# Kernel tuning notes

Measured on AMD Instinct MI355X. Metric: run time of the kernel, lower is better.

Reference implementation:

```python
import jax, jax.numpy as jnp
import numpy as np

HID = 128


def _mlp(f, W1, b1, W2, b2, W3, b3):
    h = jax.nn.relu(f @ W1 + b1)
    h = jax.nn.relu(h @ W2 + b2)
    return h @ W3 + b3


def setup_inputs() -> dict:
    key = jax.random.key(0)
    ks = jax.random.split(key, 20)
    B, T = 4096, 256
    x = jax.random.normal(ks[0], (B, T + 1, 2), dtype=jnp.float32)
    t = jax.random.uniform(ks[1], (B, 1), dtype=jnp.float32)

    def lin(k, fan_in, fan_out):
        return jax.random.normal(k, (fan_in, fan_out), jnp.float32) / jnp.sqrt(jnp.float32(fan_in))

    inp = {"x": x, "t": t}
    # forward_score MLP: input = [x_i(2), t(1), x_prev(2), n(1), path_t(2)] = 8
    inp["fw_W1"], inp["fw_b1"] = lin(ks[2], 8, HID), jnp.zeros((HID,), jnp.float32)
    inp["fw_W2"], inp["fw_b2"] = lin(ks[3], HID, HID), jnp.zeros((HID,), jnp.float32)
    inp["fw_W3"], inp["fw_b3"] = lin(ks[4], HID, 2), jnp.zeros((2,), jnp.float32)
    # backward_score MLP: input = [x_i(2), t(1), x_next(2), n(1), path_t(2)] = 8
    inp["bw_W1"], inp["bw_b1"] = lin(ks[5], 8, HID), jnp.zeros((HID,), jnp.float32)
    inp["bw_W2"], inp["bw_b2"] = lin(ks[6], HID, HID), jnp.zeros((HID,), jnp.float32)
    inp["bw_W3"], inp["bw_b3"] = lin(ks[7], HID, 2), jnp.zeros((2,), jnp.float32)
    # initial_score MLP: input = [x_0(2), t(1)] = 3
    inp["in_W1"], inp["in_b1"] = lin(ks[8], 3, HID), jnp.zeros((HID,), jnp.float32)
    inp["in_W2"], inp["in_b2"] = lin(ks[9], HID, HID), jnp.zeros((HID,), jnp.float32)
    inp["in_W3"], inp["in_b3"] = lin(ks[10], HID, 2), jnp.zeros((2,), jnp.float32)
    return inp


def reference(x, t,
              fw_W1, fw_b1, fw_W2, fw_b2, fw_W3, fw_b3,
              bw_W1, bw_b1, bw_W2, bw_b2, bw_W3, bw_b3,
              in_W1, in_b1, in_W2, in_b2, in_W3, in_b3):
    # x: [B, T+1, 2]; last slot is path_t. Equivalent of NeuralNet.get_score,
    # with the per-timestep Python loop batched across the time dimension.
    B = x.shape[0]
    T = x.shape[1] - 1  # ts_len
    x_n = x[:, :-1]                     # [B, T, 2]
    path_t = x[:, -1]                   # [B, 2]

    t_b = jnp.broadcast_to(t[:, None, :], (B, T - 1, 1))        # [B, T-1, 1]
    pt_b = jnp.broadcast_to(path_t[:, None, :], (B, T - 1, 2))  # [B, T-1, 2]

    # forward_score applied at i = 1..T-1, neighbor = x[:, i-1], n = i/T
    n_fwd = (jnp.arange(1, T, dtype=jnp.float32) / T)[None, :, None]
    n_fwd = jnp.broadcast_to(n_fwd, (B, T - 1, 1))
    fwd_feat = jnp.concatenate([x_n[:, 1:], t_b, x_n[:, :-1], n_fwd, pt_b], axis=-1)  # [B,T-1,8]
    fwd_out = _mlp(fwd_feat, fw_W1, fw_b1, fw_W2, fw_b2, fw_W3, fw_b3)                # [B,T-1,2]

    # backward_score applied at i = 0..T-2, neighbor = x[:, i+1], n = i/T
    n_bwd = (jnp.arange(0, T - 1, dtype=jnp.float32) / T)[None, :, None]
    n_bwd = jnp.broadcast_to(n_bwd, (B, T - 1, 1))
    bwd_feat = jnp.concatenate([x_n[:, :-1], t_b, x_n[:, 1:], n_bwd, pt_b], axis=-1)  # [B,T-1,8]
    bwd_out = _mlp(bwd_feat, bw_W1, bw_b1, bw_W2, bw_b2, bw_W3, bw_b3)                # [B,T-1,2]

    # initial_score at i = 0
    init_feat = jnp.concatenate([x_n[:, 0], t], axis=-1)                               # [B,3]
    init_out = _mlp(init_feat, in_W1, in_b1, in_W2, in_b2, in_W3, in_b3)               # [B,2]

    score = jnp.zeros((B, T, 2), dtype=x.dtype)
    score = score.at[:, 1:].add(fwd_out)
    score = score.at[:, :T - 1].add(bwd_out)
    score = score.at[:, 0].add(init_out)
    return score
```

## Files before the change

kernel.cpp:

```cpp
#include <hip/hip_runtime.h>
#include <stdint.h>

typedef __attribute__((ext_vector_type(8))) short short8;
typedef __attribute__((ext_vector_type(4))) float floatx4;

#define MFMA16(a, b, c) __builtin_amdgcn_mfma_f32_16x16x32_bf16(a, b, c, 0, 0, 0)

__device__ __forceinline__ unsigned short f2bf(float x) {
    unsigned u = __builtin_bit_cast(unsigned, x);
    u = (u + 0x7fffu + ((u >> 16) & 1u)) >> 16;
    return (unsigned short)u;
}

__device__ __forceinline__ int hphys(int row, int u) {
    return row * 64 + ((((u >> 2) ^ (row & 15)) << 2) | (u & 3));
}

__global__ __launch_bounds__(256)
__attribute__((amdgpu_waves_per_eu(2, 2)))
void NeuralNet_37615323578557_kernel(
        const float* __restrict__ x, const float* __restrict__ t,
        const float* __restrict__ fW1, const float* __restrict__ fb1,
        const float* __restrict__ fW2, const float* __restrict__ fb2,
        const float* __restrict__ fW3, const float* __restrict__ fb3,
        const float* __restrict__ gW1, const float* __restrict__ gb1,
        const float* __restrict__ gW2, const float* __restrict__ gb2,
        const float* __restrict__ gW3, const float* __restrict__ gb3,
        const float* __restrict__ iW1, const float* __restrict__ ib1,
        const float* __restrict__ iW2, const float* __restrict__ ib2,
        const float* __restrict__ iW3, const float* __restrict__ ib3,
        float* __restrict__ out) {
    __shared__ unsigned h1buf[128 * 64];
    __shared__ unsigned h2buf[128 * 64];
    __shared__ unsigned short fbuf[128 * 8];
    __shared__ float accT[2 * 256 * 2];

    const int tid  = threadIdx.x;
    const int lane = tid & 63;
    const int w    = tid >> 6;
    const int c    = lane & 15;
    const int q    = lane >> 4;
    const int b0   = blockIdx.x * 2;

    #pragma unroll
    for (int k = 0; k < 4; ++k) accT[tid + k * 256] = 0.0f;
    __syncthreads();

    if (w < 2) {
        float* h1s = (float*)fbuf + w * 128;
        const int b = b0 + w;
        const float* xb = x + (size_t)b * 514;
        const float f0 = xb[0], f1 = xb[1], f2 = t[b];
        const int u0 = lane, u1 = lane + 64;
        const float h0 = fmaxf(iW1[u0] * f0 + iW1[128 + u0] * f1 + iW1[256 + u0] * f2 + ib1[u0], 0.f);
        const float h1 = fmaxf(iW1[u1] * f0 + iW1[128 + u1] * f1 + iW1[256 + u1] * f2 + ib1[u1], 0.f);
        h1s[u0] = h0;
        h1s[u1] = h1;
        float a0 = ib2[lane], a1 = ib2[lane + 64];
        for (int k = 0; k < 128; ++k) {
            const float hv = h1s[k];
            a0 += hv * iW2[k * 128 + lane];
            a1 += hv * iW2[k * 128 + lane + 64];
        }
        a0 = fmaxf(a0, 0.f); a1 = fmaxf(a1, 0.f);
        float p0 = a0 * iW3[lane * 2 + 0] + a1 * iW3[(lane + 64) * 2 + 0];
        float p1 = a0 * iW3[lane * 2 + 1] + a1 * iW3[(lane + 64) * 2 + 1];
        #pragma unroll
        for (int m = 1; m < 64; m <<= 1) {
            p0 += __shfl_xor(p0, m, 64);
            p1 += __shfl_xor(p1, m, 64);
        }
        if (lane == 0) {
            accT[w * 512 + 0] += p0 + ib3[0];
            accT[w * 512 + 1] += p1 + ib3[1];
        }
    }

    const int wbase = w * 32;
    const int ucol  = w * 16 + c;

    for (int dir = 0; dir < 2; ++dir) {
        const float* W1 = dir ? gW1 : fW1;
        const float* B1 = dir ? gb1 : fb1;
        const float* W2 = dir ? gW2 : fW2;
        const float* B2 = dir ? gb2 : fb2;
        const float* W3 = dir ? gW3 : fW3;
        const float* B3 = dir ? gb3 : fb3;

        __syncthreads();

        {
            const int a  = tid >> 2;
            const int k0 = a << 1;
            const int c0 = (tid & 3) << 5;
            const int ks = k0 >> 5;
            const int q2 = (k0 >> 3) & 3;
            const int j0 = k0 & 7;
            const float* r0p = &W2[k0 * 128 + c0];
            const float* r1p = r0p + 128;
            #pragma unroll
            for (int nn = 0; nn < 32; nn += 4) {
                const float4 v0 = *(const float4*)(r0p + nn);
                const float4 v1 = *(const float4*)(r1p + nn);
                #pragma unroll
                for (int e = 0; e < 4; ++e) {
                    const int n = c0 + nn + e;
                    const unsigned pv =
                        (unsigned)f2bf(((const float*)&v0)[e]) |
                        ((unsigned)f2bf(((const float*)&v1)[e]) << 16);
                    const int B = ((n >> 5) * 2 + (n & 1)) * 4 + ks;
                    const int us = B * 512 + (q2 * 16 + ((n >> 1) & 15)) * 8 + j0;
                    h2buf[us >> 1] = pv;
                }
            }
        }

        short8 w1f[2], w3f[4];
        float  b1v[2], b2v[2];
        #pragma unroll
        for (int ntl = 0; ntl < 2; ++ntl) {
            const int col = wbase + 2 * c + ntl;
            b1v[ntl] = B1[col];
            b2v[ntl] = B2[col];
            short8 f = {0, 0, 0, 0, 0, 0, 0, 0};
            if (q == 0) {
                #pragma unroll
                for (int j = 0; j < 8; ++j) f[j] = (short)f2bf(W1[j * 128 + col]);
            }
            w1f[ntl] = f;
        }
        const float b3c = (c < 2) ? B3[c] : 0.0f;
        #pragma unroll
        for (int ks = 0; ks < 4; ++ks) {
            short8 f = {0, 0, 0, 0, 0, 0, 0, 0};
            if (c < 2) {
                #pragma unroll
                for (int j = 0; j < 8; ++j)
                    f[j] = (short)f2bf(W3[(ks * 32 + q * 8 + j) * 2 + c]);
            }
            w3f[ks] = f;
        }
        __syncthreads();

        short8 w2f[2][4];
        {
            const unsigned short* img = (const unsigned short*)h2buf;
            #pragma unroll
            for (int ntl = 0; ntl < 2; ++ntl)
                #pragma unroll
                for (int ks = 0; ks < 4; ++ks)
                    w2f[ntl][ks] = *(const short8*)
                        &img[(((w * 2 + ntl) * 4 + ks) << 9) + lane * 8];
        }

        for (int tt = 0; tt < 4; ++tt) {
            const int r0 = tt * 128;

            if (tid < 128) {
                const int r = r0 + tid;
                short8 v = {0, 0, 0, 0, 0, 0, 0, 0};
                if (r < 510) {
                    const int bl = r / 255;
                    const int i  = r - bl * 255;
                    const float* xb = x + (size_t)(b0 + bl) * 514;
                    const float2 xi  = *(const float2*)(xb + 2 * i);
                    const float2 xi1 = *(const float2*)(xb + 2 * i + 2);
                    const float2 pt  = *(const float2*)(xb + 512);
                    const float tv = t[b0 + bl];
                    const float nv = (float)(dir ? i : (i + 1)) * (1.0f / 256.0f);
                    if (dir == 0) {
                        v[0] = (short)f2bf(xi1.x); v[1] = (short)f2bf(xi1.y);
                        v[2] = (short)f2bf(tv);
                        v[3] = (short)f2bf(xi.x);  v[4] = (short)f2bf(xi.y);
                    } else {
                        v[0] = (short)f2bf(xi.x);  v[1] = (short)f2bf(xi.y);
                        v[2] = (short)f2bf(tv);
                        v[3] = (short)f2bf(xi1.x); v[4] = (short)f2bf(xi1.y);
                    }
                    v[5] = (short)f2bf(nv);
                    v[6] = (short)f2bf(pt.x); v[7] = (short)f2bf(pt.y);
                }
                *(short8*)&fbuf[tid * 8] = v;
            }
            __syncthreads();

            #pragma unroll
            for (int mt = 0; mt < 8; ++mt) {
                short8 af = {0, 0, 0, 0, 0, 0, 0, 0};
                if (q == 0) af = *(const short8*)&fbuf[(mt * 16 + c) * 8];
                floatx4 a0 = {b1v[0], b1v[0], b1v[0], b1v[0]};
                floatx4 a1 = {b1v[1], b1v[1], b1v[1], b1v[1]};
                a0 = MFMA16(af, w1f[0], a0);
                a1 = MFMA16(af, w1f[1], a1);
                const int rowb = mt * 16 + q * 4;
                #pragma unroll
                for (int rr = 0; rr < 4; ++rr) {
                    const unsigned pv = (unsigned)f2bf(fmaxf(a0[rr], 0.0f)) |
                                        ((unsigned)f2bf(fmaxf(a1[rr], 0.0f)) << 16);
                    h1buf[hphys(rowb + rr, ucol)] = pv;
                }
            }
            __syncthreads();

            #pragma unroll
            for (int mt = 0; mt < 8; ++mt) {
                const int row = mt * 16 + c;
                const int sw  = row & 15;
                const unsigned* rp = &h1buf[row * 64];
                short8 a0 = *(const short8*)&rp[(((0 + q) ^ sw) << 2)];
                short8 a1 = *(const short8*)&rp[(((4 + q) ^ sw) << 2)];
                short8 a2 = *(const short8*)&rp[(((8 + q) ^ sw) << 2)];
                short8 a3 = *(const short8*)&rp[(((12 + q) ^ sw) << 2)];
                floatx4 s0 = {b2v[0], b2v[0], b2v[0], b2v[0]};
                floatx4 s1 = {b2v[1], b2v[1], b2v[1], b2v[1]};
                s0 = MFMA16(a0, w2f[0][0], s0); s1 = MFMA16(a0, w2f[1][0], s1);
                s0 = MFMA16(a1, w2f[0][1], s0); s1 = MFMA16(a1, w2f[1][1], s1);
                s0 = MFMA16(a2, w2f[0][2], s0); s1 = MFMA16(a2, w2f[1][2], s1);
                s0 = MFMA16(a3, w2f[0][3], s0); s1 = MFMA16(a3, w2f[1][3], s1);
                const int rowb = mt * 16 + q * 4;
                #pragma unroll
                for (int rr = 0; rr < 4; ++rr) {
                    const unsigned pv = (unsigned)f2bf(fmaxf(s0[rr], 0.0f)) |
                                        ((unsigned)f2bf(fmaxf(s1[rr], 0.0f)) << 16);
                    h2buf[hphys(rowb + rr, ucol)] = pv;
                }
            }
            __syncthreads();

            #pragma unroll
            for (int mm = 0; mm < 2; ++mm) {
                const int row = w * 32 + mm * 16 + c;
                const int sw  = row & 15;
                const unsigned* rp = &h2buf[row * 64];
                short8 a0 = *(const short8*)&rp[(((0 + q) ^ sw) << 2)];
                short8 a1 = *(const short8*)&rp[(((4 + q) ^ sw) << 2)];
                short8 a2 = *(const short8*)&rp[(((8 + q) ^ sw) << 2)];
                short8 a3 = *(const short8*)&rp[(((12 + q) ^ sw) << 2)];
                floatx4 s = {b3c, b3c, b3c, b3c};
                s = MFMA16(a0, w3f[0], s);
                s = MFMA16(a1, w3f[1], s);
                s = MFMA16(a2, w3f[2], s);
                s = MFMA16(a3, w3f[3], s);
                if (c < 2) {
                    const int rowb = w * 32 + mm * 16 + q * 4;
                    #pragma unroll
                    for (int rr = 0; rr < 4; ++rr) {
                        const int r = r0 + rowb + rr;
                        if (r < 510) {
                            const int bl = r / 255;
                            const int i  = r - bl * 255;
                            const int pos = i + 1 - dir;
                            accT[(bl << 9) + pos * 2 + c] += s[rr];
                        }
                    }
                }
            }
        }
    }

    __syncthreads();
    ((float4*)(out + (size_t)b0 * 512))[tid] = ((const float4*)accT)[tid];
}

extern "C" void kernel_launch(void* const* d_in, const int* in_sizes, int n_in,
                              void* d_out, int out_size, void* d_ws, size_t ws_size,
                              hipStream_t stream) {
    (void)in_sizes; (void)n_in; (void)d_ws; (void)ws_size; (void)out_size;
    const float* x   = (const float*)d_in[0];
    const float* t   = (const float*)d_in[1];
    const float* fW1 = (const float*)d_in[2];
    const float* fb1 = (const float*)d_in[3];
    const float* fW2 = (const float*)d_in[4];
    const float* fb2 = (const float*)d_in[5];
    const float* fW3 = (const float*)d_in[6];
    const float* fb3 = (const float*)d_in[7];
    const float* gW1 = (const float*)d_in[8];
    const float* gb1 = (const float*)d_in[9];
    const float* gW2 = (const float*)d_in[10];
    const float* gb2 = (const float*)d_in[11];
    const float* gW3 = (const float*)d_in[12];
    const float* gb3 = (const float*)d_in[13];
    const float* iW1 = (const float*)d_in[14];
    const float* ib1 = (const float*)d_in[15];
    const float* iW2 = (const float*)d_in[16];
    const float* ib2 = (const float*)d_in[17];
    const float* iW3 = (const float*)d_in[18];
    const float* ib3 = (const float*)d_in[19];
    float* out = (float*)d_out;

    NeuralNet_37615323578557_kernel<<<dim3(2048), 256, 0, stream>>>(
        x, t, fW1, fb1, fW2, fb2, fW3, fb3,
        gW1, gb1, gW2, gb2, gW3, gb3,
        iW1, ib1, iW2, ib2, iW3, ib3, out);
}
```

Before: 295.6 us.

## Halve row tile and merge LDS buffers to double occupancy, cheaper bf16 packing

Shrinks the per-iteration row tile from 128 to 64 rows and lets the W2 staging image alias the h1/h2 activation buffers, cutting LDS per block roughly in half. The waves_per_eu target goes from 2 to 4 so more blocks can be resident per CU and hide latency. It also replaces the round-to-nearest-even bf16 conversion with a cheaper add-and-byte-permute packer. The cost is twice as many barrier-separated tile iterations, tighter register budgets that may spill, and slightly different rounding on ties.

```diff
diff --git a/kernel.cpp b/kernel.cpp
--- a/kernel.cpp
+++ b/kernel.cpp
@@ -6,6 +6,11 @@
 
 #define MFMA16(a, b, c) __builtin_amdgcn_mfma_f32_16x16x32_bf16(a, b, c, 0, 0, 0)
 
+__device__ __forceinline__ unsigned pkbf(float lo, float hi) {
+    const unsigned a = __builtin_bit_cast(unsigned, lo) + 0x8000u;
+    const unsigned b = __builtin_bit_cast(unsigned, hi) + 0x8000u;
+    return __builtin_amdgcn_perm(b, a, 0x07060302u);
+}
 __device__ __forceinline__ unsigned short f2bf(float x) {
     unsigned u = __builtin_bit_cast(unsigned, x);
     u = (u + 0x7fffu + ((u >> 16) & 1u)) >> 16;
@@ -17,7 +22,7 @@
 }
 
 __global__ __launch_bounds__(256)
-__attribute__((amdgpu_waves_per_eu(2, 2)))
+__attribute__((amdgpu_waves_per_eu(4, 4)))
 void NeuralNet_37615323578557_kernel(
         const float* __restrict__ x, const float* __restrict__ t,
         const float* __restrict__ fW1, const float* __restrict__ fb1,
@@ -30,10 +35,12 @@
         const float* __restrict__ iW2, const float* __restrict__ ib2,
         const float* __restrict__ iW3, const float* __restrict__ ib3,
         float* __restrict__ out) {
-    __shared__ unsigned h1buf[128 * 64];
-    __shared__ unsigned h2buf[128 * 64];
-    __shared__ unsigned short fbuf[128 * 8];
+    __shared__ unsigned sbuf[8192];
+    __shared__ unsigned short fbuf[64 * 8];
     __shared__ float accT[2 * 256 * 2];
+
+    unsigned* const h1buf = sbuf;
+    unsigned* const h2buf = sbuf + 4096;
 
     const int tid  = threadIdx.x;
     const int lane = tid & 63;
@@ -90,8 +97,7 @@
         __syncthreads();
 
         {
-            const int a  = tid >> 2;
-            const int k0 = a << 1;
+            const int k0 = (tid >> 2) << 1;
             const int c0 = (tid & 3) << 5;
             const int ks = k0 >> 5;
             const int q2 = (k0 >> 3) & 3;
@@ -105,12 +111,11 @@
                 #pragma unroll
                 for (int e = 0; e < 4; ++e) {
                     const int n = c0 + nn + e;
-                    const unsigned pv =
-                        (unsigned)f2bf(((const float*)&v0)[e]) |
-                        ((unsigned)f2bf(((const float*)&v1)[e]) << 16);
+                    const unsigned pv = pkbf(((const float*)&v0)[e],
+                                             ((const float*)&v1)[e]);
                     const int B = ((n >> 5) * 2 + (n & 1)) * 4 + ks;
                     const int us = B * 512 + (q2 * 16 + ((n >> 1) & 15)) * 8 + j0;
-                    h2buf[us >> 1] = pv;
+                    sbuf[us >> 1] = pv;
                 }
             }
         }
@@ -144,7 +149,7 @@
 
         short8 w2f[2][4];
         {
-            const unsigned short* img = (const unsigned short*)h2buf;
+            const unsigned short* img = (const unsigned short*)sbuf;
             #pragma unroll
             for (int ntl = 0; ntl < 2; ++ntl)
                 #pragma unroll
@@ -153,12 +158,12 @@
                         &img[(((w * 2 + ntl) * 4 + ks) << 9) + lane * 8];
         }
 
-        for (int tt = 0; tt < 4; ++tt) {
-            const int r0 = tt * 128;
-
-            if (tid < 128) {
+        for (int tt = 0; tt < 8; ++tt) {
+            const int r0 = tt * 64;
+
+            if (tid < 64) {
                 const int r = r0 + tid;
-                short8 v = {0, 0, 0, 0, 0, 0, 0, 0};
+                unsigned v0 = 0, v1 = 0, v2 = 0, v3 = 0;
                 if (r < 510) {
                     const int bl = r / 255;
                     const int i  = r - bl * 255;
@@ -169,23 +174,23 @@
                     const float tv = t[b0 + bl];
                     const float nv = (float)(dir ? i : (i + 1)) * (1.0f / 256.0f);
                     if (dir == 0) {
-                        v[0] = (short)f2bf(xi1.x); v[1] = (short)f2bf(xi1.y);
-                        v[2] = (short)f2bf(tv);
-                        v[3] = (short)f2bf(xi.x);  v[4] = (short)f2bf(xi.y);
+                        v0 = pkbf(xi1.x, xi1.y);
+                        v1 = pkbf(tv, xi.x);
+                        v2 = pkbf(xi.y, nv);
                     } else {
-                        v[0] = (short)f2bf(xi.x);  v[1] = (short)f2bf(xi.y);
-                        v[2] = (short)f2bf(tv);
-                        v[3] = (short)f2bf(xi1.x); v[4] = (short)f2bf(xi1.y);
+                        v0 = pkbf(xi.x, xi.y);
+                        v1 = pkbf(tv, xi1.x);
+                        v2 = pkbf(xi1.y, nv);
                     }
-                    v[5] = (short)f2bf(nv);
-                    v[6] = (short)f2bf(pt.x); v[7] = (short)f2bf(pt.y);
+                    v3 = pkbf(pt.x, pt.y);
                 }
-                *(short8*)&fbuf[tid * 8] = v;
+                unsigned* fp = (unsigned*)&fbuf[tid * 8];
+                fp[0] = v0; fp[1] = v1; fp[2] = v2; fp[3] = v3;
             }
             __syncthreads();
 
             #pragma unroll
-            for (int mt = 0; mt < 8; ++mt) {
+            for (int mt = 0; mt < 4; ++mt) {
                 short8 af = {0, 0, 0, 0, 0, 0, 0, 0};
                 if (q == 0) af = *(const short8*)&fbuf[(mt * 16 + c) * 8];
                 floatx4 a0 = {b1v[0], b1v[0], b1v[0], b1v[0]};
@@ -194,16 +199,14 @@
                 a1 = MFMA16(af, w1f[1], a1);
                 const int rowb = mt * 16 + q * 4;
                 #pragma unroll
-                for (int rr = 0; rr < 4; ++rr) {
-                    const unsigned pv = (unsigned)f2bf(fmaxf(a0[rr], 0.0f)) |
-                                        ((unsigned)f2bf(fmaxf(a1[rr], 0.0f)) << 16);
-                    h1buf[hphys(rowb + rr, ucol)] = pv;
-                }
+                for (int rr = 0; rr < 4; ++rr)
+                    h1buf[hphys(rowb + rr, ucol)] =
+                        pkbf(fmaxf(a0[rr], 0.0f), fmaxf(a1[rr], 0.0f));
             }
             __syncthreads();
 
             #pragma unroll
-            for (int mt = 0; mt < 8; ++mt) {
+            for (int mt = 0; mt < 4; ++mt) {
                 const int row = mt * 16 + c;
                 const int sw  = row & 15;
                 const unsigned* rp = &h1buf[row * 64];
@@ -219,17 +222,14 @@
                 s0 = MFMA16(a3, w2f[0][3], s0); s1 = MFMA16(a3, w2f[1][3], s1);
                 const int rowb = mt * 16 + q * 4;
                 #pragma unroll
-                for (int rr = 0; rr < 4; ++rr) {
-                    const unsigned pv = (unsigned)f2bf(fmaxf(s0[rr], 0.0f)) |
-                                        ((unsigned)f2bf(fmaxf(s1[rr], 0.0f)) << 16);
-                    h2buf[hphys(rowb + rr, ucol)] = pv;
-                }
+                for (int rr = 0; rr < 4; ++rr)
+                    h2buf[hphys(rowb + rr, ucol)] =
+                        pkbf(fmaxf(s0[rr], 0.0f), fmaxf(s1[rr], 0.0f));
             }
             __syncthreads();
 
-            #pragma unroll
-            for (int mm = 0; mm < 2; ++mm) {
-                const int row = w * 32 + mm * 16 + c;
+            {
+                const int row = w * 16 + c;
                 const int sw  = row & 15;
                 const unsigned* rp = &h2buf[row * 64];
                 short8 a0 = *(const short8*)&rp[(((0 + q) ^ sw) << 2)];
@@ -242,7 +242,7 @@
                 s = MFMA16(a2, w3f[2], s);
                 s = MFMA16(a3, w3f[3], s);
                 if (c < 2) {
-                    const int rowb = w * 32 + mm * 16 + q * 4;
+                    const int rowb = w * 16 + q * 4;
                     #pragma unroll
                     for (int rr = 0; rr < 4; ++rr) {
                         const int r = r0 + rowb + rr;
```

Measured after the change: 272.1 us. 7.9% less time.
